# Optimization experiments

Measured on AMD Instinct MI355X. Metric: run time of the kernel, lower is better.

## Reference

```python
import jax, jax.numpy as jnp
import numpy as np

SOBEL_X = jnp.array([[-1., 0., 1.], [-2., 0., 2.], [-1., 0., 1.]], dtype=jnp.float32)
SOBEL_Y = jnp.array([[-1., -2., -1.], [0., 0., 0.], [1., 2., 1.]], dtype=jnp.float32)


def _dwconv(x, k):
    # depthwise 3x3 conv, padding=1, groups=C. x: [B,C,H,W], k: [3,3]
    C = x.shape[1]
    kern = jnp.broadcast_to(k[None, None], (C, 1, 3, 3)).astype(x.dtype)
    return jax.lax.conv_general_dilated(
        x, kern, window_strides=(1, 1), padding=((1, 1), (1, 1)),
        dimension_numbers=('NCHW', 'OIHW', 'NCHW'), feature_group_count=C)


def setup_inputs() -> dict:
    key = jax.random.key(0)
    k1, _ = jax.random.split(key)
    u = jax.random.normal(k1, (16, 3, 512, 512), dtype=jnp.float32)
    theta = jnp.ones((1,), dtype=jnp.float32)
    return {"u": u, "theta": theta}


def reference(u, theta):
    # first derivatives
    ux = _dwconv(u, SOBEL_X)
    uy = _dwconv(u, SOBEL_Y)
    # second derivatives
    uxx = _dwconv(ux, SOBEL_X)
    uxy = _dwconv(ux, SOBEL_Y)
    uyy = _dwconv(uy, SOBEL_Y)
    # Gaussian curvature
    denom = (1.0 + ux * ux + uy * uy) ** 2
    G = (uxx * uyy - uxy * uxy) / (denom + 1e-6)
    # theta * u is computed but unused in the original forward (kept faithful)
    _ = theta * u
    phi_G = jnp.exp(-jnp.abs(G))
    P = phi_G * ux
    Q = phi_G * uy
    div_term = _dwconv(P, SOBEL_X) + _dwconv(Q, SOBEL_Y)
    return u + div_term
```

## Files before the change

kernel.cpp:

```cpp
#include <hip/hip_runtime.h>
#include <math.h>


#define HB   16
#define NROW (HB + 6)
#define NT   256

typedef float f4v __attribute__((ext_vector_type(4)));

#define STEP(TT, S0, S1, S2) do {                                              \
    const int Tt = (TT);                                                       \
    const float ur0 = ucen[S0][0], ur1 = ucen[S0][1],                          \
                ur2 = ucen[S0][2], ur3 = ucen[S0][3];                          \
    if (Tt < NROW) {                                                           \
               \
        float* du = Du[S0]; float* su = Su[S0];                                \
        _Pragma("unroll") for (int c = 0; c < 8; ++c) {                        \
            du[c] = pend[c+3] - pend[c+1];                                     \
            su[c] = pend[c+1] + 2.f*pend[c+2] + pend[c+3];                     \
        }                                                                      \
        ucen[S0][0] = pend[4]; ucen[S0][1] = pend[5];                          \
        ucen[S0][2] = pend[6]; ucen[S0][3] = pend[7];                          \
    }                                                                          \
    if (Tt + 1 < NROW) {                                                       \
         \
        const int gy = gy0 + Tt - 2;                                           \
        if ((unsigned)gy < (unsigned)H) {                                      \
            const float* row = uc + (long)gy * W;                              \
            const float4 va = *(const float4*)(row + ca);                      \
            const float4 vb = *(const float4*)(row + c0);                      \
            const float4 vc = *(const float4*)(row + cc);                      \
            pend[0] = inb0  ? va.x : 0.f;  pend[1]  = inb1  ? va.y : 0.f;      \
            pend[2] = inb2  ? va.z : 0.f;  pend[3]  = inb3  ? va.w : 0.f;      \
            pend[4] = vb.x;                pend[5]  = vb.y;                    \
            pend[6] = vb.z;                pend[7]  = vb.w;                    \
            pend[8] = inb8  ? vc.x : 0.f;  pend[9]  = inb9  ? vc.y : 0.f;      \
            pend[10] = inb10 ? vc.z : 0.f; pend[11] = inb11 ? vc.w : 0.f;      \
        } else {                                                               \
            _Pragma("unroll") for (int i = 0; i < 12; ++i) pend[i] = 0.f;      \
        }                                                                      \
    }                                                                          \
    if (Tt >= 2 && Tt < NROW) {                                                \
         \
        float* xr = xw[S2]; float* yr = yw[S2];                                \
        const int gy = gy0 + Tt - 4;                                           \
        if ((unsigned)gy < (unsigned)H) {                                      \
                                     \
            _Pragma("unroll") for (int c = 0; c < 8; ++c) {                    \
                const float x = Du[S1][c] + 2.f*Du[S2][c] + Du[S0][c];         \
                const float y = Su[S0][c] - Su[S1][c];                         \
                xr[c] = mU[c+2] ? x : 0.f;                                     \
                yr[c] = mU[c+2] ? y : 0.f;                                     \
            }                                                                  \
        } else {                                                               \
            _Pragma("unroll") for (int c = 0; c < 8; ++c) { xr[c]=0.f; yr[c]=0.f; } \
        }                                                                      \
    }                                                                          \
    if (Tt >= 4 && Tt < NROW) {                                                \
         \
        float* dp = dP[S1]; float* eq = eQ[S1];                                \
        const int gy = gy0 + Tt - 5;                                           \
        if ((unsigned)gy < (unsigned)H) {                                      \
            const float* xt = xw[S0];                         \
            const float* xm = xw[S1];                         \
            const float* xb = xw[S2];                         \
            const float* yt = yw[S0];                                          \
            const float* ym = yw[S1];                                          \
            const float* yb = yw[S2];                                          \
            float P[6], Q[6];                                                  \
            _Pragma("unroll") for (int c = 0; c < 6; ++c) {                    \
                const float xc = xm[c+1], yc = ym[c+1];                        \
                const float uxx = (xt[c+2]-xt[c]) + 2.f*(xm[c+2]-xm[c])        \
                                + (xb[c+2]-xb[c]);                             \
                const float uxy = (xb[c] + 2.f*xb[c+1] + xb[c+2])              \
                                - (xt[c] + 2.f*xt[c+1] + xt[c+2]);             \
                const float uyy = (yb[c] + 2.f*yb[c+1] + yb[c+2])              \
                                - (yt[c] + 2.f*yt[c+1] + yt[c+2]);             \
                const float den = 1.f + xc*xc + yc*yc;                         \
                const float Gv = (uxx*uyy - uxy*uxy)                           \
                               * __builtin_amdgcn_rcpf(den*den + 1e-6f);       \
                const float phi = __expf(-fabsf(Gv));                          \
                   \
                P[c] = phi * xc;                                               \
                Q[c] = phi * yc;                                               \
            }                                                                  \
            dp[0] = P[2]-P[0]; dp[1] = P[3]-P[1];                              \
            dp[2] = P[4]-P[2]; dp[3] = P[5]-P[3];                              \
            eq[0] = Q[0]+2.f*Q[1]+Q[2]; eq[1] = Q[1]+2.f*Q[2]+Q[3];            \
            eq[2] = Q[2]+2.f*Q[3]+Q[4]; eq[3] = Q[3]+2.f*Q[4]+Q[5];            \
        } else {                                                               \
            _Pragma("unroll") for (int c = 0; c < 4; ++c) { dp[c]=0.f; eq[c]=0.f; } \
        }                                                                      \
    }                                                                          \
    if (Tt >= 6 && Tt < NROW) {                                                \
         \
                  \
        f4v o;                                                                 \
        o.x = ur0 + (dP[S2][0] + 2.f*dP[S0][0] + dP[S1][0])                    \
                  + (eQ[S1][0] - eQ[S2][0]);                                   \
        o.y = ur1 + (dP[S2][1] + 2.f*dP[S0][1] + dP[S1][1])                    \
                  + (eQ[S1][1] - eQ[S2][1]);                                   \
        o.z = ur2 + (dP[S2][2] + 2.f*dP[S0][2] + dP[S1][2])                    \
                  + (eQ[S1][2] - eQ[S2][2]);                                   \
        o.w = ur3 + (dP[S2][3] + 2.f*dP[S0][3] + dP[S1][3])                    \
                  + (eQ[S1][3] - eQ[S2][3]);                                   \
        __builtin_nontemporal_store(o, (f4v*)(oc + (long)(gy0 + Tt - 6) * W + c0)); \
    }                                                                          \
} while (0)

__global__ __launch_bounds__(NT) void gcdd_sweep(
    const float* __restrict__ u, float* __restrict__ out, int H, int W)
{
    const int tid   = threadIdx.x;
    const int strip = tid & 127;
    const int band  = tid >> 7;
    const int c0    = strip * 4;
    const int gy0   = (blockIdx.y * 2 + band) * HB;
    const long chan = blockIdx.z;
    const float* __restrict__ uc = u + chan * (long)H * W;
    float* __restrict__ oc = out + chan * (long)H * W;

    const int ca = (c0 - 4 < 0) ? 0 : (c0 - 4);
    const int cc = (c0 + 4 > W - 4) ? (W - 4) : (c0 + 4);

    bool mU[12];
    #pragma unroll
    for (int i = 0; i < 12; ++i)
        mU[i] = (unsigned)(c0 - 4 + i) < (unsigned)W;
    const bool inb0 = mU[0], inb1 = mU[1], inb2 = mU[2], inb3 = mU[3];
    const bool inb8 = mU[8], inb9 = mU[9], inb10 = mU[10], inb11 = mU[11];

    float pend[12];
    float Du[3][8], Su[3][8];
    float ucen[3][4] = {};
    float xw[3][8], yw[3][8];
    float dP[3][4], eQ[3][4];

    {
        const int gy = gy0 - 3;
        if ((unsigned)gy < (unsigned)H) {
            const float* row = uc + (long)gy * W;
            const float4 va = *(const float4*)(row + ca);
            const float4 vb = *(const float4*)(row + c0);
            const float4 vc = *(const float4*)(row + cc);
            pend[0] = inb0  ? va.x : 0.f;  pend[1]  = inb1  ? va.y : 0.f;
            pend[2] = inb2  ? va.z : 0.f;  pend[3]  = inb3  ? va.w : 0.f;
            pend[4] = vb.x;                pend[5]  = vb.y;
            pend[6] = vb.z;                pend[7]  = vb.w;
            pend[8] = inb8  ? vc.x : 0.f;  pend[9]  = inb9  ? vc.y : 0.f;
            pend[10] = inb10 ? vc.z : 0.f; pend[11] = inb11 ? vc.w : 0.f;
        } else {
            #pragma unroll
            for (int i = 0; i < 12; ++i) pend[i] = 0.f;
        }
    }

    for (int t = 0; t < NROW + 2; t += 3) {
        STEP(t + 0, 0, 1, 2);
        STEP(t + 1, 1, 2, 0);
        STEP(t + 2, 2, 0, 1);
    }
}

extern "C" void kernel_launch(void* const* d_in, const int* in_sizes, int n_in,
                              void* d_out, int out_size, void* d_ws, size_t ws_size,
                              hipStream_t stream) {
    const float* u = (const float*)d_in[0];
    float* out = (float*)d_out;

    const int H = 512, W = 512;
    const int channels = in_sizes[0] / (H * W);

    dim3 grid(1, H / (2 * HB), channels);
    dim3 block(NT);
    gcdd_sweep<<<grid, block, 0, stream>>>(u, out, H, W);
}
```

Measured before the change: 51.43 us.

## Drop per-column boundary masks in sweep and patch image edges in a fixup kernel

```diff
diff --git a/kernel.cpp b/kernel.cpp
--- a/kernel.cpp
+++ b/kernel.cpp
@@ -2,7 +2,7 @@
 #include <math.h>
 
 
-#define HB   16
+#define HB   8
 #define NROW (HB + 6)
 #define NT   256
 
@@ -27,15 +27,9 @@
         const int gy = gy0 + Tt - 2;                                           \
         if ((unsigned)gy < (unsigned)H) {                                      \
             const float* row = uc + (long)gy * W;                              \
-            const float4 va = *(const float4*)(row + ca);                      \
-            const float4 vb = *(const float4*)(row + c0);                      \
-            const float4 vc = *(const float4*)(row + cc);                      \
-            pend[0] = inb0  ? va.x : 0.f;  pend[1]  = inb1  ? va.y : 0.f;      \
-            pend[2] = inb2  ? va.z : 0.f;  pend[3]  = inb3  ? va.w : 0.f;      \
-            pend[4] = vb.x;                pend[5]  = vb.y;                    \
-            pend[6] = vb.z;                pend[7]  = vb.w;                    \
-            pend[8] = inb8  ? vc.x : 0.f;  pend[9]  = inb9  ? vc.y : 0.f;      \
-            pend[10] = inb10 ? vc.z : 0.f; pend[11] = inb11 ? vc.w : 0.f;      \
+            *(float4*)&pend[0] = *(const float4*)(row + ca);                   \
+            *(float4*)&pend[4] = *(const float4*)(row + c0);                   \
+            *(float4*)&pend[8] = *(const float4*)(row + cc);                   \
         } else {                                                               \
             _Pragma("unroll") for (int i = 0; i < 12; ++i) pend[i] = 0.f;      \
         }                                                                      \
@@ -45,12 +39,9 @@
         float* xr = xw[S2]; float* yr = yw[S2];                                \
         const int gy = gy0 + Tt - 4;                                           \
         if ((unsigned)gy < (unsigned)H) {                                      \
-                                     \
             _Pragma("unroll") for (int c = 0; c < 8; ++c) {                    \
-                const float x = Du[S1][c] + 2.f*Du[S2][c] + Du[S0][c];         \
-                const float y = Su[S0][c] - Su[S1][c];                         \
-                xr[c] = mU[c+2] ? x : 0.f;                                     \
-                yr[c] = mU[c+2] ? y : 0.f;                                     \
+                xr[c] = Du[S1][c] + 2.f*Du[S2][c] + Du[S0][c];                 \
+                yr[c] = Su[S0][c] - Su[S1][c];                                 \
             }                                                                  \
         } else {                                                               \
             _Pragma("unroll") for (int c = 0; c < 8; ++c) { xr[c]=0.f; yr[c]=0.f; } \
@@ -80,7 +71,6 @@
                 const float Gv = (uxx*uyy - uxy*uxy)                           \
                                * __builtin_amdgcn_rcpf(den*den + 1e-6f);       \
                 const float phi = __expf(-fabsf(Gv));                          \
-                   \
                 P[c] = phi * xc;                                               \
                 Q[c] = phi * yc;                                               \
             }                                                                  \
@@ -94,7 +84,6 @@
     }                                                                          \
     if (Tt >= 6 && Tt < NROW) {                                                \
          \
-                  \
         f4v o;                                                                 \
         o.x = ur0 + (dP[S2][0] + 2.f*dP[S0][0] + dP[S1][0])                    \
                   + (eQ[S1][0] - eQ[S2][0]);                                   \
@@ -123,13 +112,6 @@
     const int ca = (c0 - 4 < 0) ? 0 : (c0 - 4);
     const int cc = (c0 + 4 > W - 4) ? (W - 4) : (c0 + 4);
 
-    bool mU[12];
-    #pragma unroll
-    for (int i = 0; i < 12; ++i)
-        mU[i] = (unsigned)(c0 - 4 + i) < (unsigned)W;
-    const bool inb0 = mU[0], inb1 = mU[1], inb2 = mU[2], inb3 = mU[3];
-    const bool inb8 = mU[8], inb9 = mU[9], inb10 = mU[10], inb11 = mU[11];
-
     float pend[12];
     float Du[3][8], Su[3][8];
     float ucen[3][4] = {};
@@ -140,26 +122,92 @@
         const int gy = gy0 - 3;
         if ((unsigned)gy < (unsigned)H) {
             const float* row = uc + (long)gy * W;
-            const float4 va = *(const float4*)(row + ca);
-            const float4 vb = *(const float4*)(row + c0);
-            const float4 vc = *(const float4*)(row + cc);
-            pend[0] = inb0  ? va.x : 0.f;  pend[1]  = inb1  ? va.y : 0.f;
-            pend[2] = inb2  ? va.z : 0.f;  pend[3]  = inb3  ? va.w : 0.f;
-            pend[4] = vb.x;                pend[5]  = vb.y;
-            pend[6] = vb.z;                pend[7]  = vb.w;
-            pend[8] = inb8  ? vc.x : 0.f;  pend[9]  = inb9  ? vc.y : 0.f;
-            pend[10] = inb10 ? vc.z : 0.f; pend[11] = inb11 ? vc.w : 0.f;
+            *(float4*)&pend[0] = *(const float4*)(row + ca);
+            *(float4*)&pend[4] = *(const float4*)(row + c0);
+            *(float4*)&pend[8] = *(const float4*)(row + cc);
         } else {
             #pragma unroll
             for (int i = 0; i < 12; ++i) pend[i] = 0.f;
         }
     }
 
-    for (int t = 0; t < NROW + 2; t += 3) {
+    for (int t = 0; t < NROW + 1; t += 3) {
         STEP(t + 0, 0, 1, 2);
         STEP(t + 1, 1, 2, 0);
         STEP(t + 2, 2, 0, 1);
     }
+}
+
+__global__ __launch_bounds__(256) void gcdd_fix(
+    const float* __restrict__ u, float* __restrict__ out, int H, int W, int CH)
+{
+    const int idx = blockIdx.x * 256 + threadIdx.x;
+    if (idx >= 6 * H * CH) return;
+    const int gy = idx % H;
+    const int t  = idx / H;
+    const int cs = t % 6;
+    const int ch = t / 6;
+    const int gx = (cs < 3) ? cs : (W - 6 + cs);
+    const float* __restrict__ uc = u + (long)ch * H * W;
+    float* __restrict__ oc = out + (long)ch * H * W;
+
+    float uv[7][7];
+    #pragma unroll
+    for (int r = 0; r < 7; ++r) {
+        const int ry = gy - 3 + r;
+        const bool ri = (unsigned)ry < (unsigned)H;
+        const int ryc = ri ? ry : 0;
+        #pragma unroll
+        for (int c = 0; c < 7; ++c) {
+            const int cx = gx - 3 + c;
+            const bool ci = (unsigned)cx < (unsigned)W;
+            const int cxc = ci ? cx : 0;
+            const float v = uc[(long)ryc * W + cxc];
+            uv[r][c] = (ri & ci) ? v : 0.f;
+        }
+    }
+    float ux[5][5], uy[5][5];
+    #pragma unroll
+    for (int r = 0; r < 5; ++r) {
+        const bool ri = (unsigned)(gy - 2 + r) < (unsigned)H;
+        #pragma unroll
+        for (int c = 0; c < 5; ++c) {
+            const bool in = ri & ((unsigned)(gx - 2 + c) < (unsigned)W);
+            const float A = uv[r][c],   B = uv[r][c+1],   C = uv[r][c+2];
+            const float D = uv[r+1][c],                   E = uv[r+1][c+2];
+            const float F = uv[r+2][c], G = uv[r+2][c+1], Hh = uv[r+2][c+2];
+            const float x = (C - A) + 2.f*(E - D) + (Hh - F);
+            const float y = (F + 2.f*G + Hh) - (A + 2.f*B + C);
+            ux[r][c] = in ? x : 0.f;
+            uy[r][c] = in ? y : 0.f;
+        }
+    }
+    float P[3][3], Q[3][3];
+    #pragma unroll
+    for (int r = 0; r < 3; ++r) {
+        const bool ri = (unsigned)(gy - 1 + r) < (unsigned)H;
+        #pragma unroll
+        for (int c = 0; c < 3; ++c) {
+            const bool in = ri & ((unsigned)(gx - 1 + c) < (unsigned)W);
+            const float xc = ux[r+1][c+1], yc = uy[r+1][c+1];
+            const float uxx = (ux[r][c+2]-ux[r][c]) + 2.f*(ux[r+1][c+2]-ux[r+1][c])
+                            + (ux[r+2][c+2]-ux[r+2][c]);
+            const float uxy = (ux[r+2][c] + 2.f*ux[r+2][c+1] + ux[r+2][c+2])
+                            - (ux[r][c]   + 2.f*ux[r][c+1]   + ux[r][c+2]);
+            const float uyy = (uy[r+2][c] + 2.f*uy[r+2][c+1] + uy[r+2][c+2])
+                            - (uy[r][c]   + 2.f*uy[r][c+1]   + uy[r][c+2]);
+            const float den = 1.f + xc*xc + yc*yc;
+            const float Gv = (uxx*uyy - uxy*uxy)
+                           * __builtin_amdgcn_rcpf(den*den + 1e-6f);
+            const float phi = __expf(-fabsf(Gv));
+            P[r][c] = in ? phi * xc : 0.f;
+            Q[r][c] = in ? phi * yc : 0.f;
+        }
+    }
+    const float divx = (P[0][2]-P[0][0]) + 2.f*(P[1][2]-P[1][0]) + (P[2][2]-P[2][0]);
+    const float divy = (Q[2][0] + 2.f*Q[2][1] + Q[2][2])
+                     - (Q[0][0] + 2.f*Q[0][1] + Q[0][2]);
+    oc[(long)gy * W + gx] = uv[3][3] + divx + divy;
 }
 
 extern "C" void kernel_launch(void* const* d_in, const int* in_sizes, int n_in,
@@ -172,6 +220,8 @@
     const int channels = in_sizes[0] / (H * W);
 
     dim3 grid(1, H / (2 * HB), channels);
-    dim3 block(NT);
-    gcdd_sweep<<<grid, block, 0, stream>>>(u, out, H, W);
+    gcdd_sweep<<<grid, dim3(NT), 0, stream>>>(u, out, H, W);
+
+    const int nfix = 6 * H * channels;
+    gcdd_fix<<<(nfix + 255) / 256, 256, 0, stream>>>(u, out, H, W, channels);
 }
```

Result: slower. 71.64 us (+39.3%).
